# Performance work log

Hardware: AMD Instinct MI355X
Metric: run time of the kernel (lower is better)

## Reference

```python
import jax, jax.numpy as jnp
import numpy as np

BETA = 0.25  # commitment loss weight


def setup_inputs() -> dict:
    key = jax.random.key(0)
    k1, k2 = jax.random.split(key)
    B, D, H, W = 16, 256, 64, 64
    K = 2048  # num_codebook
    z = jax.random.normal(k1, (B, D, H, W), dtype=jnp.float32)
    # matches nn.Embedding init uniform_(-1/K, 1/K) in scale-free way; values irrelevant to math
    codebook = jax.random.uniform(k2, (K, D), dtype=jnp.float32,
                                  minval=-1.0 / K, maxval=1.0 / K)
    return {"z": z, "codebook": codebook}


def reference(z, codebook):
    # z: (B, D, H, W) -> (B, H, W, D) -> (N, D)
    b, d, h, w = z.shape
    k = codebook.shape[0]
    z_flat = jnp.transpose(z, (0, 2, 3, 1)).reshape(-1, d)  # (N, D)

    # squared L2 distance via sum-of-squares + matmul (same expansion as torch code)
    distance = (jnp.sum(z_flat * z_flat, axis=1, keepdims=True)
                + jnp.sum(codebook * codebook, axis=1)
                - 2.0 * jnp.matmul(z_flat, codebook.T))  # (N, K)
    vq_indices = jnp.argmin(distance, axis=1)  # (N,)
    z_quantized = codebook[vq_indices]  # (N, D) gather

    # one-hot counting (scatter-add, equivalent to sum of one-hot)
    vq_current_count = jnp.zeros((k,), dtype=jnp.int32).at[vq_indices].add(1)

    sg = jax.lax.stop_gradient
    codebook_loss = jnp.mean((z_quantized - sg(z_flat)) ** 2)
    commitment_loss = jnp.mean((z_flat - sg(z_quantized)) ** 2)
    loss = codebook_loss + BETA * commitment_loss

    # straight-through estimator
    z_st = z_flat + sg(z_quantized - z_flat)
    q = jnp.transpose(z_st.reshape(b, h, w, d), (0, 3, 1, 2))  # (B, D, H, W)
    return q, loss, codebook_loss, commitment_loss, vq_current_count
```

## Files before the change

### kernel.cpp

```cpp
#include <hip/hip_runtime.h>

#define N_TOT 65536
#define K_CB  2048
#define D_DIM 256
#define HW    4096
#define DHW   1048576

typedef _Float16 half8 __attribute__((ext_vector_type(8)));
typedef _Float16 half4v __attribute__((ext_vector_type(4)));
typedef float f32x16 __attribute__((ext_vector_type(16)));


__device__ __forceinline__ void gload_lds16(const void* g, void* l) {
    __builtin_amdgcn_global_load_lds((const __attribute__((address_space(1))) void*)g,
                                     (__attribute__((address_space(3))) void*)l, 16, 0, 0);
}

__device__ __forceinline__ float pw128_sq(const float* __restrict__ base, int stride) {
    #pragma clang fp contract(off)
    float r[8];
    #pragma unroll
    for (int j = 0; j < 8; ++j) { float v = base[j * stride]; r[j] = v * v; }
    for (int i = 8; i < 128; i += 8) {
        #pragma unroll
        for (int j = 0; j < 8; ++j) { float v = base[(i + j) * stride]; r[j] += v * v; }
    }
    return ((r[0] + r[1]) + (r[2] + r[3])) + ((r[4] + r[5]) + (r[6] + r[7]));
}

__global__ void cbnorm_zero_kernel(const float* __restrict__ cb, float* __restrict__ cb2,
                                   int* __restrict__ counts, float* __restrict__ sse) {
    #pragma clang fp contract(off)
    int k = blockIdx.x * 256 + threadIdx.x;
    const float* row = cb + (size_t)k * D_DIM;
    cb2[k] = pw128_sq(row, 1) + pw128_sq(row + 128, 1);
    counts[k] = 0;
    if (k == 0) *sse = 0.f;
}

__global__ void split_c_kernel(const float* __restrict__ cb,
                               _Float16* __restrict__ ch, _Float16* __restrict__ cl) {
    int e = (blockIdx.x * 256 + threadIdx.x) * 4;
    float4 v = *(const float4*)(cb + e);
    float xs[4] = {v.x, v.y, v.z, v.w};
    half4v hh, hl;
    #pragma unroll
    for (int u = 0; u < 4; ++u) {
        float x = xs[u] * 16384.0f;
        _Float16 hv = (_Float16)x;
        hh[u] = hv;
        hl[u] = (_Float16)(x - (float)hv);
    }
    *(half4v*)(ch + e) = hh;
    *(half4v*)(cl + e) = hl;
}

__global__ void fused_z_kernel(const float* __restrict__ z,
                               _Float16* __restrict__ zh, _Float16* __restrict__ zl,
                               float* __restrict__ z2,
                               unsigned long long* __restrict__ rowmin_g) {
    __shared__ __align__(16) float lt[256 * 33];
    __shared__ float rj[512];
    __shared__ float hh[64];
    int t = threadIdx.x;
    int n0 = blockIdx.x * 32;
    int b = n0 >> 12, s0 = n0 & 4095;
    const float* zb = z + (size_t)b * DHW + s0;

    #pragma unroll
    for (int v = 0; v < 8; ++v) {
        int f = v * 256 + t;
        int d = f >> 3, nch = f & 7;
        float4 val = *(const float4*)(zb + (size_t)d * HW + nch * 4);
        lt[d * 33 + nch * 4 + 0] = val.x;
        lt[d * 33 + nch * 4 + 1] = val.y;
        lt[d * 33 + nch * 4 + 2] = val.z;
        lt[d * 33 + nch * 4 + 3] = val.w;
    }
    __syncthreads();

    {
        #pragma clang fp contract(off)
        int n = t & 31, j = t >> 5;
        #pragma unroll
        for (int hf = 0; hf < 2; ++hf) {
            float r = 0.f;
            #pragma unroll
            for (int i = 0; i < 16; ++i) {
                float v = lt[(hf * 128 + i * 8 + j) * 33 + n];
                r += v * v;
            }
            rj[n * 16 + hf * 8 + j] = r;
        }
    }

    #pragma unroll
    for (int v = 0; v < 8; ++v) {
        int g = v * 256 + t;
        int n = g >> 6, du = g & 63;
        half4v hv, lv;
        #pragma unroll
        for (int u = 0; u < 4; ++u) {
            float x = lt[(du * 4 + u) * 33 + n] * 2048.0f;
            _Float16 h = (_Float16)x;
            hv[u] = h;
            lv[u] = (_Float16)(x - (float)h);
        }
        size_t off = (size_t)(n0 + n) * 256 + du * 4;
        *(half4v*)(zh + off) = hv;
        *(half4v*)(zl + off) = lv;
    }
    __syncthreads();

    if (t < 64) {
        #pragma clang fp contract(off)
        int n = t & 31, hf = t >> 5;
        const float* r = &rj[n * 16 + hf * 8];
        hh[hf * 32 + n] = ((r[0] + r[1]) + (r[2] + r[3])) + ((r[4] + r[5]) + (r[6] + r[7]));
    }
    __syncthreads();
    if (t < 32) {
        #pragma clang fp contract(off)
        z2[n0 + t] = hh[t] + hh[32 + t];
        rowmin_g[n0 + t] = ~0ull;
    }
}


__device__ __forceinline__ unsigned long long kmin_xor(unsigned long long key, int m) {
    unsigned lo = (unsigned)key, hi = (unsigned)(key >> 32);
    unsigned olo = __shfl_xor(lo, m);
    unsigned ohi = __shfl_xor(hi, m);
    unsigned long long o = ((unsigned long long)ohi << 32) | olo;
    return (o < key) ? o : key;
}

__launch_bounds__(256, 4)
__global__ void argmin_mfma_kernel(const _Float16* __restrict__ zh, const _Float16* __restrict__ zl,
                                   const _Float16* __restrict__ ch, const _Float16* __restrict__ cl,
                                   const float* __restrict__ cb2, const float* __restrict__ z2arr,
                                   unsigned long long* __restrict__ rowmin_g) {
    __shared__ __align__(16) char lds_raw[32768];
    _Float16* lds_a = (_Float16*)lds_raw;
    _Float16* lds_b = (_Float16*)(lds_raw + 16384);

    int t = threadIdx.x;
    int bid = blockIdx.x;
    int swz = (bid & 7) * 1024 + (bid >> 3);
    int r0 = (swz >> 4) * 128;
    int c0 = (swz & 15) * 128;
    int w = t >> 6, lane = t & 63;
    int wm = w >> 1, wn = w & 1;
    int l31 = lane & 31, l5 = lane >> 5;

    f32x16 acc[2][2];
    #pragma unroll
    for (int i = 0; i < 2; ++i)
        #pragma unroll
        for (int j = 0; j < 2; ++j)
            #pragma unroll
            for (int r = 0; r < 16; ++r) acc[i][j][r] = 0.f;

    float c2v[2];
    #pragma unroll
    for (int j = 0; j < 2; ++j)
        c2v[j] = cb2[c0 + wn * 64 + j * 32 + l31];

    for (int ki = 0; ki < 12; ++ki) {
        int seg  = ki >> 2;
        int koff = (ki & 3) * 64;
        const _Float16* asrc = (seg < 2) ? zh : zl;
        const _Float16* bsrc = (seg == 1) ? cl : ch;
        __syncthreads();
        #pragma unroll
        for (int v = 0; v < 4; ++v) {
            int p = v * 256 + t;
            int row = p >> 3;
            int ku = (p & 7) ^ (row & 7);
            gload_lds16(asrc + (size_t)((r0 + row) * 256 + koff + ku * 8), lds_a + p * 8);
        }
        #pragma unroll
        for (int v = 0; v < 4; ++v) {
            int p = v * 256 + t;
            int row = p >> 3;
            int ku = (p & 7) ^ (row & 7);
            gload_lds16(bsrc + (size_t)((c0 + row) * 256 + koff + ku * 8), lds_b + p * 8);
        }
        __syncthreads();
        #pragma unroll
        for (int ks = 0; ks < 4; ++ks) {
            half8 af[2], bf[2];
            #pragma unroll
            for (int i = 0; i < 2; ++i) {
                int row = wm * 64 + i * 32 + l31;
                int ku  = (ks * 2 + l5) ^ (row & 7);
                af[i] = *(const half8*)(lds_a + row * 64 + ku * 8);
            }
            #pragma unroll
            for (int j = 0; j < 2; ++j) {
                int row = wn * 64 + j * 32 + l31;
                int ku  = (ks * 2 + l5) ^ (row & 7);
                bf[j] = *(const half8*)(lds_b + row * 64 + ku * 8);
            }
            #pragma unroll
            for (int i = 0; i < 2; ++i)
                #pragma unroll
                for (int j = 0; j < 2; ++j)
                    acc[i][j] = __builtin_amdgcn_mfma_f32_32x32x16_f16(af[i], bf[j], acc[i][j], 0, 0, 0);
        }
    }
    __syncthreads();

    unsigned long long* scratch = (unsigned long long*)lds_raw;
    #pragma unroll
    for (int i = 0; i < 2; ++i) {
        #pragma unroll
        for (int rg = 0; rg < 16; ++rg) {
            int rowoff = (rg & 3) + 8 * (rg >> 2) + 4 * l5;
            int m = wm * 64 + i * 32 + rowoff;
            float zz = z2arr[r0 + m];
            unsigned long long key = ~0ull;
            #pragma unroll
            for (int j = 0; j < 2; ++j) {
                float sc = (zz + c2v[j]) - acc[i][j][rg] * (1.0f / 16777216.0f);
                unsigned long long k2 = ((unsigned long long)__float_as_uint(sc) << 32)
                                      | (unsigned)(c0 + wn * 64 + j * 32 + l31);
                key = (k2 < key) ? k2 : key;
            }
            key = kmin_xor(key, 16);
            key = kmin_xor(key, 8);
            if (l31 < 8) scratch[m * 18 + wn * 8 + l31] = key;
        }
    }
    __syncthreads();
    if (t < 128) {
        const ulonglong2* srow = (const ulonglong2*)(scratch + t * 18);
        unsigned long long best = ~0ull;
        #pragma unroll
        for (int s = 0; s < 8; ++s) {
            ulonglong2 p = srow[s];
            if (p.x < best) best = p.x;
            if (p.y < best) best = p.y;
        }
        atomicMin(&rowmin_g[r0 + t], best);
    }
}

__global__ void gather_kernel(const float* __restrict__ z, const float* __restrict__ cb,
                              const unsigned long long* __restrict__ rowmin_g,
                              float* __restrict__ qout,
                              float* __restrict__ sse, int* __restrict__ counts) {
    int t = threadIdx.x;
    int si = t & 63, dg = t >> 6;
    int n = blockIdx.x * 64 + si;
    int idx = (int)(rowmin_g[n] & 0xFFFFFFFFull);
    int b = n >> 12, s = n & 4095;
    const float* zb = z + (size_t)b * DHW + s;
    float*       qb = qout + (size_t)b * DHW + s;
    const float4* crow = (const float4*)(cb + (size_t)idx * D_DIM + dg * 64);
    float acc = 0.f;
    #pragma unroll
    for (int dd4 = 0; dd4 < 16; ++dd4) {
        float4 q4 = crow[dd4];
        float qv[4] = {q4.x, q4.y, q4.z, q4.w};
        #pragma unroll
        for (int u = 0; u < 4; ++u) {
            int d = dg * 64 + dd4 * 4 + u;
            float zv = zb[(size_t)d * HW];
            qb[(size_t)d * HW] = qv[u];
            float df = zv - qv[u];
            acc += df * df;
        }
    }
    #pragma unroll
    for (int off = 32; off > 0; off >>= 1) acc += __shfl_down(acc, off, 64);
    if ((t & 63) == 0) atomicAdd(sse, acc);
    if (dg == 0) atomicAdd(&counts[idx], 1);
}

__global__ void finalize_kernel(const float* __restrict__ sse, const int* __restrict__ counts,
                                float* __restrict__ out) {
    int t = threadIdx.x;
    float mse = *sse * (1.0f / 16777216.0f);
    if (t == 0) {
        out[16777216] = mse * 1.25f;
        out[16777217] = mse;
        out[16777218] = mse;
    }
    for (int i = t; i < 2048; i += 256) out[16777219 + i] = (float)counts[i];
}

extern "C" void kernel_launch(void* const* d_in, const int* in_sizes, int n_in,
                              void* d_out, int out_size, void* d_ws, size_t ws_size,
                              hipStream_t stream) {
    const float* z  = (const float*)d_in[0];
    const float* cb = (const float*)d_in[1];
    float* out = (float*)d_out;
    float* ws  = (float*)d_ws;

    float* cb2    = ws;
    int*   counts = (int*)(ws + 2048);
    float* sse    = ws + 4096;
    float* z2     = ws + 4352;
    unsigned long long* rowmin_g = (unsigned long long*)(ws + 69888);
    _Float16* ch  = (_Float16*)(ws + 200960);
    _Float16* cl  = (_Float16*)(ws + 463104);

    _Float16* zzh = (_Float16*)d_out;
    _Float16* zzl = zzh + 16777216;

    cbnorm_zero_kernel<<<8, 256, 0, stream>>>(cb, cb2, counts, sse);
    split_c_kernel<<<512, 256, 0, stream>>>(cb, ch, cl);
    fused_z_kernel<<<2048, 256, 0, stream>>>(z, zzh, zzl, z2, rowmin_g);
    argmin_mfma_kernel<<<8192, 256, 0, stream>>>(zzh, zzl, ch, cl, cb2, z2, rowmin_g);
    gather_kernel<<<1024, 256, 0, stream>>>(z, cb, rowmin_g, out, sse, counts);
    finalize_kernel<<<1, 256, 0, stream>>>(sse, counts, out);
}
```

Before: 453.9 us.

## Double-buffer B tile in LDS and load A fragments directly to registers

Restructures the argmin MFMA main loop into a two-stage software pipeline. The codebook (B) tile is double-buffered in LDS while the z (A) fragments are loaded straight from global memory into registers and double-buffered there, with manual waitcnt and barriers so the next tile's loads overlap the current tile's MFMAs. This cuts the two full syncthreads per k-step and the A LDS round-trip. In exchange, register pressure rises, so launch bounds drop from 4 to 3 blocks per CU. The A global loads are also no longer coalesced through LDS, and the hand-written vmcnt counts are fragile.

```diff
diff --git a/kernel.cpp b/kernel.cpp
--- a/kernel.cpp
+++ b/kernel.cpp
@@ -135,14 +135,14 @@
     return (o < key) ? o : key;
 }
 
-__launch_bounds__(256, 4)
+__launch_bounds__(256, 3)
 __global__ void argmin_mfma_kernel(const _Float16* __restrict__ zh, const _Float16* __restrict__ zl,
                                    const _Float16* __restrict__ ch, const _Float16* __restrict__ cl,
                                    const float* __restrict__ cb2, const float* __restrict__ z2arr,
                                    unsigned long long* __restrict__ rowmin_g) {
     __shared__ __align__(16) char lds_raw[32768];
-    _Float16* lds_a = (_Float16*)lds_raw;
-    _Float16* lds_b = (_Float16*)(lds_raw + 16384);
+    _Float16* b0 = (_Float16*)lds_raw;
+    _Float16* b1 = (_Float16*)(lds_raw + 16384);
 
     int t = threadIdx.x;
     int bid = blockIdx.x;
@@ -166,48 +166,73 @@
     for (int j = 0; j < 2; ++j)
         c2v[j] = cb2[c0 + wn * 64 + j * 32 + l31];
 
-    for (int ki = 0; ki < 12; ++ki) {
-        int seg  = ki >> 2;
-        int koff = (ki & 3) * 64;
-        const _Float16* asrc = (seg < 2) ? zh : zl;
-        const _Float16* bsrc = (seg == 1) ? cl : ch;
-        __syncthreads();
+    int arow0 = r0 + wm * 64 + l31;
+    int arow1 = arow0 + 32;
+    int akoff = l5 * 8;
+
+    auto stage_B = [&](int kt, _Float16* nb) {
+        const _Float16* bsrc = ((kt >> 2) == 1) ? cl : ch;
+        int koff = (kt & 3) * 64;
         #pragma unroll
         for (int v = 0; v < 4; ++v) {
             int p = v * 256 + t;
             int row = p >> 3;
             int ku = (p & 7) ^ (row & 7);
-            gload_lds16(asrc + (size_t)((r0 + row) * 256 + koff + ku * 8), lds_a + p * 8);
-        }
-        #pragma unroll
-        for (int v = 0; v < 4; ++v) {
-            int p = v * 256 + t;
-            int row = p >> 3;
-            int ku = (p & 7) ^ (row & 7);
-            gload_lds16(bsrc + (size_t)((c0 + row) * 256 + koff + ku * 8), lds_b + p * 8);
-        }
-        __syncthreads();
+            gload_lds16(bsrc + (size_t)((c0 + row) * 256 + koff + ku * 8), nb + p * 8);
+        }
+    };
+    auto load_A = [&](int kt, half8 (&dst)[2][4]) {
+        const _Float16* as = (kt < 8) ? zh : zl;
+        int ko = (kt & 3) * 64 + akoff;
         #pragma unroll
         for (int ks = 0; ks < 4; ++ks) {
-            half8 af[2], bf[2];
-            #pragma unroll
-            for (int i = 0; i < 2; ++i) {
-                int row = wm * 64 + i * 32 + l31;
-                int ku  = (ks * 2 + l5) ^ (row & 7);
-                af[i] = *(const half8*)(lds_a + row * 64 + ku * 8);
-            }
+            dst[0][ks] = *(const half8*)(as + (size_t)arow0 * 256 + ko + ks * 16);
+            dst[1][ks] = *(const half8*)(as + (size_t)arow1 * 256 + ko + ks * 16);
+        }
+    };
+    auto compute = [&](const _Float16* lb, const half8 (&af)[2][4]) {
+        #pragma unroll
+        for (int ks = 0; ks < 4; ++ks) {
+            half8 bf[2];
             #pragma unroll
             for (int j = 0; j < 2; ++j) {
                 int row = wn * 64 + j * 32 + l31;
                 int ku  = (ks * 2 + l5) ^ (row & 7);
-                bf[j] = *(const half8*)(lds_b + row * 64 + ku * 8);
+                bf[j] = *(const half8*)(lb + row * 64 + ku * 8);
             }
             #pragma unroll
             for (int i = 0; i < 2; ++i)
                 #pragma unroll
                 for (int j = 0; j < 2; ++j)
-                    acc[i][j] = __builtin_amdgcn_mfma_f32_32x32x16_f16(af[i], bf[j], acc[i][j], 0, 0, 0);
-        }
+                    acc[i][j] = __builtin_amdgcn_mfma_f32_32x32x16_f16(af[i][ks], bf[j], acc[i][j], 0, 0, 0);
+        }
+    };
+
+    half8 afA[2][4], afB[2][4];
+
+    stage_B(0, b0);
+    load_A(0, afA);
+    __syncthreads();
+
+    #pragma unroll 1
+    for (int kp = 0; kp < 6; ++kp) {
+        int kt1 = kp * 2 + 1;
+        stage_B(kt1, b1);
+        __builtin_amdgcn_sched_barrier(0);
+        load_A(kt1, afB);
+        compute(b0, afA);
+        asm volatile("s_waitcnt lgkmcnt(0)" ::: "memory");
+        asm volatile("s_waitcnt vmcnt(8)" ::: "memory");
+        __builtin_amdgcn_s_barrier();
+        if (kp < 5) {
+            stage_B(kt1 + 1, b0);
+            __builtin_amdgcn_sched_barrier(0);
+            load_A(kt1 + 1, afA);
+        }
+        compute(b1, afB);
+        asm volatile("s_waitcnt lgkmcnt(0)" ::: "memory");
+        asm volatile("s_waitcnt vmcnt(8)" ::: "memory");
+        __builtin_amdgcn_s_barrier();
     }
     __syncthreads();
 
```

New measurement: 651.7 us. 1.44x slower.
